# Kernel tuning notes

Hardware: AMD Instinct MI355X
Metric: run time of the kernel (lower is better)

## Reference

```python
import jax, jax.numpy as jnp
import numpy as np

C = 256          # channels
G = 4            # groups
K = 3            # kernel_size
P = K * K        # sampling points per group
GC = C // G      # group channels
PAD = (K - 1) // 2
OFFSET_SCALE = 1.0


def setup_inputs() -> dict:
    key = jax.random.key(0)
    ks = jax.random.split(key, 6)
    N, H, W = 2, 96, 96
    x = jax.random.normal(ks[0], (N, C, H, W), jnp.float32)
    uncertainty_map = jax.random.uniform(ks[1], (N, 1, H, W), jnp.float32)
    # depthwise conv params (Conv2d groups=C -> weight [C,1,K,K])
    dw_w = jax.random.normal(ks[2], (C, 1, K, K), jnp.float32) * 0.05
    dw_b = jax.random.normal(ks[3], (C,), jnp.float32) * 0.05
    # GroupNorm(1, C) affine params
    gn_w = jnp.ones((C,), jnp.float32)
    gn_b = jnp.zeros((C,), jnp.float32)
    # offset/mask linear: [G*K*K*3, C] (module inits to zero; use small random for a nontrivial test)
    om_w = jax.random.normal(ks[4], (G * P * 3, C), jnp.float32) * 0.01
    om_b = jax.random.normal(ks[5], (G * P * 3,), jnp.float32) * 0.01
    return dict(x=x, uncertainty_map=uncertainty_map, dw_w=dw_w, dw_b=dw_b,
                gn_w=gn_w, gn_b=gn_b, om_w=om_w, om_b=om_b)


def _dcn_forward(x, uncertainty_map, dw_w, dw_b, gn_w, gn_b, om_w, om_b):
    N, C_, H, W = x.shape
    # ---- depthwise conv + GroupNorm(1,C) + GELU context ----
    ctx = jax.lax.conv_general_dilated(
        x, dw_w, window_strides=(1, 1), padding=[(PAD, PAD), (PAD, PAD)],
        dimension_numbers=('NCHW', 'OIHW', 'NCHW'), feature_group_count=C_)
    ctx = ctx + dw_b[None, :, None, None]
    mu = ctx.mean(axis=(1, 2, 3), keepdims=True)
    var = ((ctx - mu) ** 2).mean(axis=(1, 2, 3), keepdims=True)
    ctx = (ctx - mu) * jax.lax.rsqrt(var + 1e-5)
    ctx = ctx * gn_w[None, :, None, None] + gn_b[None, :, None, None]
    ctx = jax.nn.gelu(ctx, approximate=False)
    feat = ctx.transpose(0, 2, 3, 1)                       # [N,H,W,C]
    # ---- offset / mask heads ----
    om = feat @ om_w.T + om_b                              # [N,H,W,G*P*3]
    off = om[..., : G * P * 2].reshape(N, H, W, G, P, 2)   # (dx,dy) pairs
    mask = om[..., G * P * 2:].reshape(N, H, W, G, P)
    mask = jax.nn.softmax(mask, axis=-1)
    u = uncertainty_map.transpose(0, 2, 3, 1)[..., None]   # [N,H,W,1,1]
    mask = mask * u
    # ---- DCNv3 sampling (stride=1, dilation=1, pad=(K-1)//2) ----
    x_in = x.transpose(0, 2, 3, 1)                         # NHWC
    Hp, Wp = H + 2 * PAD, W + 2 * PAD
    x_pad = jnp.pad(x_in, ((0, 0), (PAD, PAD), (PAD, PAD), (0, 0)))
    x_pad = x_pad.reshape(N, Hp, Wp, G, GC)
    # reference points normalized by padded size (align with dcnv3_core_pytorch)
    base = (K - 1) / 2 + 0.5
    ref_x = (base + jnp.arange(W, dtype=jnp.float32)) / Wp
    ref_y = (base + jnp.arange(H, dtype=jnp.float32)) / Hp
    ref = jnp.stack(jnp.broadcast_arrays(ref_x[None, :], ref_y[:, None]), axis=-1)  # [H,W,2]
    # dilation grid: x-major point ordering, (x,y) normalized
    gpts = jnp.arange(K, dtype=jnp.float32) - (K - 1) // 2
    px = jnp.repeat(gpts, K)
    py = jnp.tile(gpts, K)
    grid = jnp.stack([px / Wp, py / Hp], axis=-1)          # [P,2]
    norm = jnp.array([Wp, Hp], jnp.float32)
    loc = (ref[None, :, :, None, None, :] + grid[None, None, None, None, :, :] * OFFSET_SCALE
           + off * (OFFSET_SCALE / norm))                  # [N,H,W,G,P,2] in [0,1] of padded
    # grid_sample align_corners=False: pixel = loc*size - 0.5
    sx = loc[..., 0] * Wp - 0.5
    sy = loc[..., 1] * Hp - 0.5

    def sample_one(img, ys, xs):
        # img [Hp,Wp,GC]; ys/xs [H,W,P] -> [H,W,P,GC]
        y0 = jnp.floor(ys); x0 = jnp.floor(xs)
        wy = ys - y0; wx = xs - x0
        y0i = y0.astype(jnp.int32); x0i = x0.astype(jnp.int32)
        def gather(yi, xi):
            valid = (yi >= 0) & (yi < Hp) & (xi >= 0) & (xi < Wp)
            yc = jnp.clip(yi, 0, Hp - 1); xc = jnp.clip(xi, 0, Wp - 1)
            return img[yc, xc] * valid[..., None].astype(img.dtype)
        v00 = gather(y0i, x0i);     v01 = gather(y0i, x0i + 1)
        v10 = gather(y0i + 1, x0i); v11 = gather(y0i + 1, x0i + 1)
        return (v00 * ((1 - wy) * (1 - wx))[..., None] + v01 * ((1 - wy) * wx)[..., None]
                + v10 * (wy * (1 - wx))[..., None] + v11 * (wy * wx)[..., None])

    sample_g = jax.vmap(sample_one, in_axes=(2, 2, 2), out_axes=2)     # over groups
    sampled = jax.vmap(sample_g, in_axes=(0, 0, 0))(x_pad, sy, sx)     # [N,H,W,G,P,GC]
    out = jnp.einsum('nhwgpc,nhwgp->nhwgc', sampled, mask).reshape(N, H, W, C_)
    return out.transpose(0, 3, 1, 2)                       # [N,C,H,W]


def reference(x, uncertainty_map, dw_w, dw_b, gn_w, gn_b, om_w, om_b):
    return _dcn_forward(x, uncertainty_map, dw_w, dw_b, gn_w, gn_b, om_w, om_b)
```

## Files before the change

kernel.cpp:

```cpp
#include <hip/hip_runtime.h>
#include <hip/hip_bf16.h>
#include <hip/hip_fp16.h>
#include <math.h>

#define C_   256
#define G_   4
#define P_   9
#define GC_  64
#define H_   96
#define W_   96
#define N_   2
#define HW_  (H_*W_)
#define CHW_ (C_*H_*W_)
#define OMC  108
#define OMR  112
#define TILE 16
#define NBW  (W_/TILE)
#define NBLK (N_*H_*NBW)
#define NCONV 1536
#define NOMW  16
#define R_ST  99
#define C_ST  (3*R_ST)
#define FEATB_ST 264
#define OMS_ST 114
#define TBUF_ST 17

typedef __attribute__((ext_vector_type(8))) short bf16x8;
typedef __attribute__((ext_vector_type(4))) float f32x4;

__device__ __forceinline__ short f2bf(float f) {
    __hip_bfloat16 h = __float2bfloat16(f);
    return *reinterpret_cast<short*>(&h);
}


__global__ __launch_bounds__(256) void prep_kernel(
    const float* __restrict__ x, const float* __restrict__ dw_w,
    const float* __restrict__ dw_b, const float* __restrict__ om_w,
    __hip_bfloat16* __restrict__ xn, __hip_bfloat16* __restrict__ ctx,
    __hip_bfloat16* __restrict__ omwb, float* __restrict__ partials)
{
    const int b = blockIdx.x;
    const int tid = threadIdx.x;

    if (b >= NCONV) {
        const int bb = b - NCONV;
        const float4* src = (const float4*)om_w;
        ushort4* dst = (ushort4*)omwb;
#pragma unroll
        for (int it = 0; it < 2; ++it) {
            int i = tid + it * 256;
            if (i < 448) {
                int fi = bb * 448 + i;
                float4 v = (fi < 6912) ? src[fi] : make_float4(0.f, 0.f, 0.f, 0.f);
                ushort4 u;
                u.x = (unsigned short)f2bf(v.x); u.y = (unsigned short)f2bf(v.y);
                u.z = (unsigned short)f2bf(v.z); u.w = (unsigned short)f2bf(v.w);
                dst[fi] = u;
            }
        }
        return;
    }

    __shared__ float xs[32 * C_ST];
    __shared__ float red[8];
    const int xcd = b & 7, i = b >> 3;
    const int nh = xcd * 24 + (i >> 3);
    const int ct = i & 7;
    const int n = nh / H_, h = nh % H_;
    const int c0 = ct * 32;

    if (tid < 96) {
        int c = tid / 3, r = tid % 3;
        xs[c * C_ST + r * R_ST + 0] = 0.0f;
        xs[c * C_ST + r * R_ST + 97] = 0.0f;
    }
#pragma unroll
    for (int it = 0; it < 9; ++it) {
        int idx = tid + it * 256;
        int row = idx / 24;
        int col = idx % 24;
        int c = row / 3, r = row % 3;
        int gy = h - 1 + r;
        float4 v = make_float4(0.f, 0.f, 0.f, 0.f);
        if (gy >= 0 && gy < H_)
            v = *(const float4*)&x[(size_t)(n * C_ + c0 + c) * HW_ + gy * W_ + col * 4];
        float* dstp = &xs[c * C_ST + r * R_ST + 1 + col * 4];
        dstp[0] = v.x; dstp[1] = v.y; dstp[2] = v.z; dstp[3] = v.w;
    }
    __syncthreads();

    const int c = tid & 31, wslot = tid >> 5;
    const int W0 = wslot * 12;
    float wgt[9];
#pragma unroll
    for (int q = 0; q < 9; ++q) wgt[q] = dw_w[(c0 + c) * 9 + q];
    const float bias = dw_b[c0 + c];

    float seg[3][14];
#pragma unroll
    for (int r = 0; r < 3; ++r)
#pragma unroll
        for (int k = 0; k < 14; ++k)
            seg[r][k] = xs[c * C_ST + r * R_ST + W0 + k];

    __hip_bfloat16* cb = ctx + ((size_t)nh * W_ + W0) * C_ + c0 + c;
    __hip_bfloat16* xb = xn  + ((size_t)nh * W_ + W0) * C_ + c0 + c;
    float s1 = 0.0f, s2 = 0.0f;
#pragma unroll
    for (int j = 0; j < 12; ++j) {
        float v = bias;
#pragma unroll
        for (int r = 0; r < 3; ++r)
            v += wgt[r * 3 + 0] * seg[r][j]
               + wgt[r * 3 + 1] * seg[r][j + 1]
               + wgt[r * 3 + 2] * seg[r][j + 2];
        s1 += v; s2 += v * v;
        cb[j * C_] = __float2bfloat16(v);
        xb[j * C_] = __float2bfloat16(seg[1][j + 1]);
    }
#pragma unroll
    for (int off = 32; off; off >>= 1) {
        s1 += __shfl_down(s1, off, 64);
        s2 += __shfl_down(s2, off, 64);
    }
    const int lane = tid & 63, wv = tid >> 6;
    if (lane == 0) { red[wv] = s1; red[4 + wv] = s2; }
    __syncthreads();
    if (tid == 0) {
        partials[b * 2 + 0] = red[0] + red[1] + red[2] + red[3];
        partials[b * 2 + 1] = red[4] + red[5] + red[6] + red[7];
    }
}

__global__ __launch_bounds__(256) void stats_kernel(
    const float* __restrict__ partials, float* __restrict__ stats)
{
    const int tid = threadIdx.x;
    float a0 = 0, b0 = 0, a1 = 0, b1 = 0;
#pragma unroll
    for (int it = 0; it < 6; ++it) {
        int i = tid + it * 256;
        float p1 = partials[i * 2 + 0], p2 = partials[i * 2 + 1];
        if (((i & 7) >> 2) == 0) { a0 += p1; b0 += p2; }
        else                     { a1 += p1; b1 += p2; }
    }
#pragma unroll
    for (int off = 32; off; off >>= 1) {
        a0 += __shfl_down(a0, off, 64); b0 += __shfl_down(b0, off, 64);
        a1 += __shfl_down(a1, off, 64); b1 += __shfl_down(b1, off, 64);
    }
    __shared__ float red[4][4];
    const int lane = tid & 63, wv = tid >> 6;
    if (lane == 0) { red[wv][0] = a0; red[wv][1] = b0; red[wv][2] = a1; red[wv][3] = b1; }
    __syncthreads();
    if (tid == 0) {
        float A0 = red[0][0] + red[1][0] + red[2][0] + red[3][0];
        float B0 = red[0][1] + red[1][1] + red[2][1] + red[3][1];
        float A1 = red[0][2] + red[1][2] + red[2][2] + red[3][2];
        float B1 = red[0][3] + red[1][3] + red[2][3] + red[3][3];
        float m0 = A0 * (1.0f / (float)CHW_);
        float v0 = B0 * (1.0f / (float)CHW_) - m0 * m0;
        float m1 = A1 * (1.0f / (float)CHW_);
        float v1 = B1 * (1.0f / (float)CHW_) - m1 * m1;
        stats[0] = m0; stats[1] = rsqrtf(v0 + 1e-5f);
        stats[2] = m1; stats[3] = rsqrtf(v1 + 1e-5f);
    }
}

__global__ __launch_bounds__(256, 5) void main_kernel(
    const __hip_bfloat16* __restrict__ xn, const float* __restrict__ unc,
    const __hip_bfloat16* __restrict__ ctx, const float* __restrict__ stats,
    const float* __restrict__ gn_w, const float* __restrict__ gn_b,
    const __hip_bfloat16* __restrict__ omwb, const float* __restrict__ om_b,
    float* __restrict__ out)
{
    __shared__ __align__(16) char smem[31232];
    short* featb  = (short*)smem;
    uint2* tidx   = (uint2*)smem;
    float4* twt   = (float4*)(smem + 4608);
    float* oms    = (float*)(smem + 13824);
    float* tbuf   = (float*)(smem + 13824);

    const int tid = threadIdx.x;
    const int b = blockIdx.x;
    const int xcd = b & 7, bidx = b >> 3;
    const int tile = xcd * (NBLK / 8) + bidx;
    const int n = tile / (H_ * NBW);
    const int rem = tile % (H_ * NBW);
    const int h = rem / NBW;
    const int w0 = (rem % NBW) * TILE;

    {
        const int c = tid;
        const float mean = stats[n * 2 + 0];
        const float rstd = stats[n * 2 + 1];
        const float gw = gn_w[c], gb = gn_b[c];
        const __hip_bfloat16* cb = ctx + ((size_t)(n * H_ + h) * W_ + w0) * C_ + c;
#pragma unroll
        for (int j = 0; j < TILE; ++j) {
            float v = __bfloat162float(cb[j * C_]);
            float f = (v - mean) * rstd * gw + gb;
            f = 0.5f * f * (1.0f + erff(f * 0.70710678118654752f));
            featb[j * FEATB_ST + c] = f2bf(f);
        }
    }
    __syncthreads();

    {
        const int wv = tid >> 6, lane = tid & 63;
        const int mrow = lane & 15, quad = lane >> 4;
        const short* fb  = featb + mrow * FEATB_ST;
        const short* wb0 = (const short*)omwb + (wv * 16 + mrow) * 256;
        const short* wb1 = (const short*)omwb + ((wv + 4) * 16 + mrow) * 256;
        f32x4 acc0 = {0.f, 0.f, 0.f, 0.f}, acc1 = {0.f, 0.f, 0.f, 0.f};
#pragma unroll
        for (int ks = 0; ks < 8; ++ks) {
            const int k = ks * 32 + quad * 8;
            bf16x8 a  = *(const bf16x8*)(fb + k);
            bf16x8 b0 = *(const bf16x8*)(wb0 + k);
            acc0 = __builtin_amdgcn_mfma_f32_16x16x32_bf16(a, b0, acc0, 0, 0, 0);
            if (wv < 3) {
                bf16x8 b1 = *(const bf16x8*)(wb1 + k);
                acc1 = __builtin_amdgcn_mfma_f32_16x16x32_bf16(a, b1, acc1, 0, 0, 0);
            }
        }
        const int j0 = wv * 16 + mrow;
        const float ob0 = om_b[j0];
#pragma unroll
        for (int rg = 0; rg < 4; ++rg)
            oms[(quad * 4 + rg) * OMS_ST + j0] = acc0[rg] + ob0;
        if (wv < 3) {
            const int j1 = (wv + 4) * 16 + mrow;
            if (j1 < OMC) {
                const float ob1 = om_b[j1];
#pragma unroll
                for (int rg = 0; rg < 4; ++rg)
                    oms[(quad * 4 + rg) * OMS_ST + j1] = acc1[rg] + ob1;
            }
        }
    }
    __syncthreads();

    if (tid < TILE * G_) {
        int pix = tid >> 2, g = tid & 3;
        float* m = &oms[pix * OMS_ST + G_ * P_ * 2 + g * P_];
        float mx = m[0];
#pragma unroll
        for (int p = 1; p < P_; ++p) mx = fmaxf(mx, m[p]);
        float e[P_], s = 0.0f;
#pragma unroll
        for (int p = 0; p < P_; ++p) { e[p] = expf(m[p] - mx); s += e[p]; }
        float u = unc[(n * H_ + h) * W_ + w0 + pix];
        float inv = u / s;
#pragma unroll
        for (int p = 0; p < P_; ++p) m[p] = e[p] * inv;
    }
    __syncthreads();

    for (int e = tid; e < TILE * G_ * P_; e += 256) {
        int pix = e / (G_ * P_);
        int rr = e - pix * (G_ * P_);
        int g = rr / P_, p = rr - g * P_;
        const float* po = &oms[pix * OMS_ST];
        float ox = po[(g * P_ + p) * 2 + 0];
        float oy = po[(g * P_ + p) * 2 + 1];
        float mk = po[G_ * P_ * 2 + g * P_ + p];
        float sx = (float)(w0 + pix + p / 3) + ox;
        float sy = (float)(h + p % 3) + oy;
        float x0f = floorf(sx), y0f = floorf(sy);
        float wx = sx - x0f, wy = sy - y0f;
        int x0 = (int)x0f - 1, y0 = (int)y0f - 1;
        float fy0 = (y0 >= 0 && y0 < H_) ? 1.0f : 0.0f;
        float fy1 = (y0 + 1 >= 0 && y0 + 1 < H_) ? 1.0f : 0.0f;
        float fx0 = (x0 >= 0 && x0 < W_) ? 1.0f : 0.0f;
        float fx1 = (x0 + 1 >= 0 && x0 + 1 < W_) ? 1.0f : 0.0f;
        int y0c = min(max(y0, 0), H_ - 1), y1c = min(max(y0 + 1, 0), H_ - 1);
        int x0c = min(max(x0, 0), W_ - 1), x1c = min(max(x0 + 1, 0), W_ - 1);
        unsigned i00 = (unsigned)(y0c * W_ + x0c), i01 = (unsigned)(y0c * W_ + x1c);
        unsigned i10 = (unsigned)(y1c * W_ + x0c), i11 = (unsigned)(y1c * W_ + x1c);
        tidx[e] = make_uint2(i00 | (i01 << 16), i10 | (i11 << 16));
        twt[e] = make_float4((1.0f - wy) * (1.0f - wx) * mk * fy0 * fx0,
                             (1.0f - wy) * wx * mk * fy0 * fx1,
                             wy * (1.0f - wx) * mk * fy1 * fx0,
                             wy * wx * mk * fy1 * fx1);
    }
    __syncthreads();

    {
        const int g = tid >> 6;
        const int lane = tid & 63;
        const __hip_bfloat16* xg = xn + (size_t)n * HW_ * C_ + g * GC_ + lane;
#pragma unroll 1
        for (int pix = 0; pix < TILE; ++pix) {
            const int te = pix * (G_ * P_) + g * P_;
            float acc = 0.0f;
#pragma unroll
            for (int p = 0; p < P_; ++p) {
                uint2 bi = tidx[te + p];
                float4 wt = twt[te + p];
                acc += wt.x * __bfloat162float(xg[(bi.x & 0xffffu) << 8])
                     + wt.y * __bfloat162float(xg[(bi.x >> 16) << 8])
                     + wt.z * __bfloat162float(xg[(bi.y & 0xffffu) << 8])
                     + wt.w * __bfloat162float(xg[(bi.y >> 16) << 8]);
            }
            tbuf[(g * GC_ + lane) * TBUF_ST + pix] = acc;
        }
    }
    __syncthreads();

    {
        const int px = tid & 15, c0 = tid >> 4;
        float* op = out + (size_t)n * CHW_ + (size_t)h * W_ + w0 + px;
#pragma unroll
        for (int k = 0; k < 16; ++k) {
            int c = c0 * 16 + k;
            op[(size_t)c * HW_] = tbuf[c * TBUF_ST + px];
        }
    }
}

extern "C" void kernel_launch(void* const* d_in, const int* in_sizes, int n_in,
                              void* d_out, int out_size, void* d_ws, size_t ws_size,
                              hipStream_t stream)
{
    const float* x    = (const float*)d_in[0];
    const float* unc  = (const float*)d_in[1];
    const float* dw_w = (const float*)d_in[2];
    const float* dw_b = (const float*)d_in[3];
    const float* gn_w = (const float*)d_in[4];
    const float* gn_b = (const float*)d_in[5];
    const float* om_w = (const float*)d_in[6];
    const float* om_b = (const float*)d_in[7];
    float* out = (float*)d_out;

    float* partials      = (float*)d_ws;
    float* stats         = (float*)((char*)d_ws + 12288);
    __hip_bfloat16* omwb = (__hip_bfloat16*)((char*)d_ws + 16384);
    __hip_bfloat16* xn   = (__hip_bfloat16*)((char*)d_ws + 81920);
    __hip_bfloat16* ctx  = xn + (size_t)N_ * HW_ * C_;

    prep_kernel<<<NCONV + NOMW, 256, 0, stream>>>(x, dw_w, dw_b, om_w, xn, ctx, omwb, partials);
    stats_kernel<<<1, 256, 0, stream>>>(partials, stats);
    main_kernel<<<NBLK, 256, 0, stream>>>(xn, unc, ctx, stats,
                                          gn_w, gn_b, omwb, om_b, out);
}
```

Measured before the change: 139.8 us.

## Tile depthwise conv over 4 rows x 16 channels with bf16 shared staging

The prep kernel now has each block process 4 output rows for 16 channels instead of 1 row for 32 channels. It loads a 6-row halo once, so the 3-row halo reloads drop from 3x to 1.5x per output row. Input is converted to bf16 before it is stored in shared memory, which halves the LDS footprint and lets each thread read packed pairs. The cost is that the conv now reads bf16-rounded inputs, which changes numerics slightly, and the stats kernel's partial count and its even/odd batch split rely on the new block indexing.

```diff
diff --git a/kernel.cpp b/kernel.cpp
--- a/kernel.cpp
+++ b/kernel.cpp
@@ -17,10 +17,10 @@
 #define TILE 16
 #define NBW  (W_/TILE)
 #define NBLK (N_*H_*NBW)
-#define NCONV 1536
+#define NCONV 768
 #define NOMW  16
-#define R_ST  99
-#define C_ST  (3*R_ST)
+#define CH_ST 628
+#define ROW_ST 104
 #define FEATB_ST 264
 #define OMS_ST 114
 #define TBUF_ST 17
@@ -31,6 +31,15 @@
 __device__ __forceinline__ short f2bf(float f) {
     __hip_bfloat16 h = __float2bfloat16(f);
     return *reinterpret_cast<short*>(&h);
+}
+__device__ __forceinline__ unsigned short f2bfu(float f) {
+    return (unsigned short)f2bf(f);
+}
+__device__ __forceinline__ float bflo(unsigned u) {
+    union { unsigned q; float f; } v; v.q = u << 16; return v.f;
+}
+__device__ __forceinline__ float bfhi(unsigned u) {
+    union { unsigned q; float f; } v; v.q = u & 0xffff0000u; return v.f;
 }
 
 
@@ -54,70 +63,96 @@
                 int fi = bb * 448 + i;
                 float4 v = (fi < 6912) ? src[fi] : make_float4(0.f, 0.f, 0.f, 0.f);
                 ushort4 u;
-                u.x = (unsigned short)f2bf(v.x); u.y = (unsigned short)f2bf(v.y);
-                u.z = (unsigned short)f2bf(v.z); u.w = (unsigned short)f2bf(v.w);
+                u.x = f2bfu(v.x); u.y = f2bfu(v.y);
+                u.z = f2bfu(v.z); u.w = f2bfu(v.w);
                 dst[fi] = u;
             }
         }
         return;
     }
 
-    __shared__ float xs[32 * C_ST];
+    __shared__ short xs[16 * CH_ST];
     __shared__ float red[8];
-    const int xcd = b & 7, i = b >> 3;
-    const int nh = xcd * 24 + (i >> 3);
-    const int ct = i & 7;
-    const int n = nh / H_, h = nh % H_;
-    const int c0 = ct * 32;
+    const int xcd = b & 7, q = b >> 3;
+    const int nh4 = xcd * 6 + (q >> 4);
+    const int ct = q & 15;
+    const int n = nh4 / 24, h0 = (nh4 % 24) * 4;
+    const int c0 = ct * 16;
 
     if (tid < 96) {
-        int c = tid / 3, r = tid % 3;
-        xs[c * C_ST + r * R_ST + 0] = 0.0f;
-        xs[c * C_ST + r * R_ST + 97] = 0.0f;
-    }
-#pragma unroll
-    for (int it = 0; it < 9; ++it) {
-        int idx = tid + it * 256;
-        int row = idx / 24;
-        int col = idx % 24;
-        int c = row / 3, r = row % 3;
-        int gy = h - 1 + r;
-        float4 v = make_float4(0.f, 0.f, 0.f, 0.f);
-        if (gy >= 0 && gy < H_)
-            v = *(const float4*)&x[(size_t)(n * C_ + c0 + c) * HW_ + gy * W_ + col * 4];
-        float* dstp = &xs[c * C_ST + r * R_ST + 1 + col * 4];
-        dstp[0] = v.x; dstp[1] = v.y; dstp[2] = v.z; dstp[3] = v.w;
-    }
-    __syncthreads();
-
-    const int c = tid & 31, wslot = tid >> 5;
-    const int W0 = wslot * 12;
+        int c = tid / 6, r = tid % 6;
+        unsigned* zp = (unsigned*)xs;
+        zp[c * (CH_ST / 2) + r * (ROW_ST / 2) + 1]  = 0u;
+        zp[c * (CH_ST / 2) + r * (ROW_ST / 2) + 50] = 0u;
+    }
+    {
+        ushort4* xsv = (ushort4*)xs;
+#pragma unroll
+        for (int it = 0; it < 9; ++it) {
+            int idx = tid + it * 256;
+            int row = idx / 24;
+            int col4 = idx % 24;
+            int c = row / 6, r = row % 6;
+            int gy = h0 - 1 + r;
+            ushort4 u = make_ushort4(0, 0, 0, 0);
+            if (gy >= 0 && gy < H_) {
+                float4 v = *(const float4*)&x[(size_t)(n * C_ + c0 + c) * HW_ + gy * W_ + col4 * 4];
+                u.x = f2bfu(v.x); u.y = f2bfu(v.y);
+                u.z = f2bfu(v.z); u.w = f2bfu(v.w);
+            }
+            xsv[c * (CH_ST / 4) + r * (ROW_ST / 4) + 1 + col4] = u;
+        }
+    }
+    __syncthreads();
+
+    const int c = tid & 15;
+    const int slot = tid >> 4;
+    const int jr = slot >> 3;
+    const int ws = slot & 7;
+    const int W0 = ws * 12;
     float wgt[9];
 #pragma unroll
-    for (int q = 0; q < 9; ++q) wgt[q] = dw_w[(c0 + c) * 9 + q];
+    for (int kq = 0; kq < 9; ++kq) wgt[kq] = dw_w[(c0 + c) * 9 + kq];
     const float bias = dw_b[c0 + c];
 
-    float seg[3][14];
-#pragma unroll
-    for (int r = 0; r < 3; ++r)
-#pragma unroll
-        for (int k = 0; k < 14; ++k)
-            seg[r][k] = xs[c * C_ST + r * R_ST + W0 + k];
-
-    __hip_bfloat16* cb = ctx + ((size_t)nh * W_ + W0) * C_ + c0 + c;
-    __hip_bfloat16* xb = xn  + ((size_t)nh * W_ + W0) * C_ + c0 + c;
     float s1 = 0.0f, s2 = 0.0f;
 #pragma unroll
-    for (int j = 0; j < 12; ++j) {
-        float v = bias;
-#pragma unroll
-        for (int r = 0; r < 3; ++r)
-            v += wgt[r * 3 + 0] * seg[r][j]
-               + wgt[r * 3 + 1] * seg[r][j + 1]
-               + wgt[r * 3 + 2] * seg[r][j + 2];
-        s1 += v; s2 += v * v;
-        cb[j * C_] = __float2bfloat16(v);
-        xb[j * C_] = __float2bfloat16(seg[1][j + 1]);
+    for (int jj = 0; jj < 2; ++jj) {
+        const int j = jr * 2 + jj;
+        float acc[12];
+#pragma unroll
+        for (int px = 0; px < 12; ++px) acc[px] = bias;
+        float xnv[12];
+#pragma unroll
+        for (int r3 = 0; r3 < 3; ++r3) {
+            const unsigned* rp = (const unsigned*)xs
+                               + c * (CH_ST / 2) + (j + r3) * (ROW_ST / 2) + 6 * ws + 1;
+            float vals[16];
+#pragma unroll
+            for (int i = 0; i < 8; ++i) {
+                unsigned u = rp[i];
+                vals[2 * i]     = bflo(u);
+                vals[2 * i + 1] = bfhi(u);
+            }
+            const float w0v = wgt[r3 * 3 + 0], w1v = wgt[r3 * 3 + 1], w2v = wgt[r3 * 3 + 2];
+#pragma unroll
+            for (int px = 0; px < 12; ++px)
+                acc[px] += w0v * vals[px + 1] + w1v * vals[px + 2] + w2v * vals[px + 3];
+            if (r3 == 1) {
+#pragma unroll
+                for (int px = 0; px < 12; ++px) xnv[px] = vals[px + 2];
+            }
+        }
+        const int gh = h0 + j;
+        __hip_bfloat16* cb = ctx + ((size_t)(n * H_ + gh) * W_ + W0) * C_ + c0 + c;
+        __hip_bfloat16* xb = xn  + ((size_t)(n * H_ + gh) * W_ + W0) * C_ + c0 + c;
+#pragma unroll
+        for (int px = 0; px < 12; ++px) {
+            float v = acc[px];
+            s1 += v; s2 += v * v;
+            cb[px * C_] = __float2bfloat16(v);
+            xb[px * C_] = __float2bfloat16(xnv[px]);
+        }
     }
 #pragma unroll
     for (int off = 32; off; off >>= 1) {
@@ -139,7 +174,7 @@
     const int tid = threadIdx.x;
     float a0 = 0, b0 = 0, a1 = 0, b1 = 0;
 #pragma unroll
-    for (int it = 0; it < 6; ++it) {
+    for (int it = 0; it < 3; ++it) {
         int i = tid + it * 256;
         float p1 = partials[i * 2 + 0], p2 = partials[i * 2 + 1];
         if (((i & 7) >> 2) == 0) { a0 += p1; b0 += p2; }
```

Measured after the change: 138.3 us. No clear change (-1.1%).
